# Kernel optimization log

Measured on AMD Instinct MI355X. Metric: run time of the kernel, lower is better.

The kernel has to match this reference:

```python
import jax, jax.numpy as jnp
import numpy as np

N, E, B = 20000, 320000, 64          # nodes, edges (before self-loops), graphs
IN_D, HID, HEADS, OUT_D = 768, 128, 4, 256
H1 = HID * HEADS                      # 512, concat output of first two GAT layers


def setup_inputs() -> dict:
    key = jax.random.key(0)
    ks = jax.random.split(key, 16)
    g = lambda k, shape, fan: jax.random.normal(k, shape, jnp.float32) * (1.0 / np.sqrt(fan))
    x = jax.random.normal(ks[0], (N, IN_D), jnp.float32)
    edge_index = jax.random.randint(ks[1], (2, E), 0, N)
    batch = jnp.sort(jax.random.randint(ks[2], (N,), 0, B))
    return {
        "x": x, "edge_index": edge_index, "batch": batch,
        # layer 1: in 768 -> 4 heads x 128, concat
        "W1": g(ks[3], (IN_D, H1), IN_D), "a_src1": g(ks[4], (HEADS, HID), HID),
        "a_dst1": g(ks[5], (HEADS, HID), HID), "b1": jnp.zeros((H1,), jnp.float32),
        "gamma1": jnp.ones((H1,), jnp.float32), "beta1": jnp.zeros((H1,), jnp.float32),
        # layer 2: in 512 -> 4 heads x 128, concat
        "W2": g(ks[6], (H1, H1), H1), "a_src2": g(ks[7], (HEADS, HID), HID),
        "a_dst2": g(ks[8], (HEADS, HID), HID), "b2": jnp.zeros((H1,), jnp.float32),
        "gamma2": jnp.ones((H1,), jnp.float32), "beta2": jnp.zeros((H1,), jnp.float32),
        # layer 3: in 512 -> 1 head x 256, no concat
        "W3": g(ks[9], (H1, OUT_D), H1), "a_src3": g(ks[10], (1, OUT_D), OUT_D),
        "a_dst3": g(ks[11], (1, OUT_D), OUT_D), "b3": jnp.zeros((OUT_D,), jnp.float32),
    }


def _gat(h_in, src, dst, W, a_s, a_d, b, heads, out_ch, concat):
    """PyG-style GATConv (shared src/dst weight, leaky_relu(0.2) attention)."""
    n = h_in.shape[0]
    h = (h_in @ W).reshape(n, heads, out_ch)                       # [N,H,C]
    e = jax.nn.leaky_relu(jnp.sum(h * a_s, -1)[src] + jnp.sum(h * a_d, -1)[dst], 0.2)  # [E,H]
    m = jax.ops.segment_max(e, dst, num_segments=n)                # stable segment softmax over dst
    p = jnp.exp(e - m[dst])
    alpha = p / (jax.ops.segment_sum(p, dst, num_segments=n)[dst] + 1e-16)
    out = jax.ops.segment_sum(h[src] * alpha[:, :, None], dst, num_segments=n)  # [N,H,C]
    out = out.reshape(n, heads * out_ch) if concat else out.mean(1)
    return out + b


def _bn(x, gamma, beta):
    mu = jnp.mean(x, axis=0)
    var = jnp.var(x, axis=0)
    return gamma * (x - mu) / jnp.sqrt(var + 1e-5) + beta


def reference(x, edge_index, batch,
              W1, a_src1, a_dst1, b1, gamma1, beta1,
              W2, a_src2, a_dst2, b2, gamma2, beta2,
              W3, a_src3, a_dst3, b3):
    loops = jnp.arange(N, dtype=edge_index.dtype)                  # PyG adds self-loops
    src = jnp.concatenate([edge_index[0], loops])
    dst = jnp.concatenate([edge_index[1], loops])
    h = _gat(x, src, dst, W1, a_src1, a_dst1, b1, HEADS, HID, True)
    h = jax.nn.leaky_relu(_bn(h, gamma1, beta1), 0.2)
    h = _gat(h, src, dst, W2, a_src2, a_dst2, b2, HEADS, HID, True)
    h = jax.nn.leaky_relu(_bn(h, gamma2, beta2), 0.2)
    h = jax.nn.leaky_relu(_gat(h, src, dst, W3, a_src3, a_dst3, b3, 1, OUT_D, False), 0.2)
    # global mean pool per graph
    sums = jax.ops.segment_sum(h, batch, num_segments=B)           # [B,OUT_D]
    cnt = jax.ops.segment_sum(jnp.ones((N, 1), h.dtype), batch, num_segments=B)
    return sums / jnp.maximum(cnt, 1.0)
```

## Files before the change

### kernel.cpp

```cpp
#include <hip/hip_runtime.h>
#include <hip/hip_bf16.h>

typedef __hip_bfloat16 bf16;
#define DEV __device__ __forceinline__

using short8 = __attribute__((ext_vector_type(8))) short;
using f32x4  = __attribute__((ext_vector_type(4))) float;

constexpr int NN   = 20000;
constexpr int NE   = 320000;
constexpr int ET   = NE + NN;
constexpr int NB   = 64;
constexpr int IND  = 768;
constexpr int HID  = 128;
constexpr int NH   = 4;
constexpr int H1   = 512;
constexpr int OUTD = 256;
constexpr int NBLK = (NN + 255) / 256;

DEV float b2f(bf16 v) { return __bfloat162float(v); }
DEV bf16  f2b(float v) { return __float2bfloat16(v); }
DEV short f2bs(float v) { bf16 h = __float2bfloat16(v); return *reinterpret_cast<short*>(&h); }
DEV float us2f(unsigned short u) { bf16 h; *reinterpret_cast<unsigned short*>(&h) = u; return __bfloat162float(h); }
DEV float lrelu(float x) { return x > 0.f ? x : 0.2f * x; }

DEV short8 load8(const bf16* p) { return *reinterpret_cast<const short8*>(p); }
DEV short8 load8(const float* p) {
  const float4 a = *reinterpret_cast<const float4*>(p);
  const float4 b = *reinterpret_cast<const float4*>(p + 4);
  short8 r;
  r[0] = f2bs(a.x); r[1] = f2bs(a.y); r[2] = f2bs(a.z); r[3] = f2bs(a.w);
  r[4] = f2bs(b.x); r[5] = f2bs(b.y); r[6] = f2bs(b.z); r[7] = f2bs(b.w);
  return r;
}

__global__ __launch_bounds__(256) void wt_kernel(
    const float* __restrict__ W, bf16* __restrict__ wt, int K, int N)
{
  __shared__ float tile[32][33];
  const int k0 = blockIdx.x * 32;
  const int n0 = blockIdx.y * 32;
  const int tx = threadIdx.x & 31;
  const int ty0 = threadIdx.x >> 5;
  for (int ty = ty0; ty < 32; ty += 8)
    tile[ty][tx] = W[(size_t)(k0 + ty) * N + n0 + tx];
  __syncthreads();
  for (int ty = ty0; ty < 32; ty += 8)
    wt[(size_t)(n0 + ty) * K + k0 + tx] = f2b(tile[tx][ty]);
}

template <typename T>
__global__ __launch_bounds__(256) void gemm_mfma(
    const T* __restrict__ A, const bf16* __restrict__ Wt,
    bf16* __restrict__ C, int M, int K, int N)
{
  __shared__ char lds[2 * 128 * 64 * 2];
  char* Asw = lds;
  char* Bsw = lds + 16384;
  const int t    = threadIdx.x;
  const int lane = t & 63;
  const int wid  = t >> 6;
  const int wr   = wid >> 1, wc = wid & 1;
  const int brow = blockIdx.x * 128;
  const int bcol = blockIdx.y * 128;
  const int l15  = lane & 15;
  const int kq   = (lane >> 4) * 8;

  f32x4 acc[4][4];
#pragma unroll
  for (int m = 0; m < 4; ++m)
#pragma unroll
    for (int n = 0; n < 4; ++n) acc[m][n] = (f32x4){0.f, 0.f, 0.f, 0.f};

  for (int kt = 0; kt < K; kt += 64) {
#pragma unroll
    for (int i = 0; i < 4; ++i) {
      const int idx = i * 256 + t;
      const int row = idx >> 3;
      const int k8  = (idx & 7) * 8;
      const int woff = (row * 128 + k8 * 2) ^ ((row & 7) << 4);
      short8 av = {0, 0, 0, 0, 0, 0, 0, 0};
      if (brow + row < M) av = load8(A + (size_t)(brow + row) * K + kt + k8);
      *reinterpret_cast<short8*>(Asw + woff) = av;
      const short8 bv = load8(Wt + (size_t)(bcol + row) * K + kt + k8);
      *reinterpret_cast<short8*>(Bsw + woff) = bv;
    }
    __syncthreads();
#pragma unroll
    for (int kk = 0; kk < 2; ++kk) {
      short8 a[4], b[4];
#pragma unroll
      for (int m = 0; m < 4; ++m) {
        const int r = wr * 64 + m * 16 + l15;
        const int k = kk * 32 + kq;
        a[m] = *reinterpret_cast<const short8*>(Asw + ((r * 128 + k * 2) ^ ((r & 7) << 4)));
      }
#pragma unroll
      for (int n = 0; n < 4; ++n) {
        const int r = wc * 64 + n * 16 + l15;
        const int k = kk * 32 + kq;
        b[n] = *reinterpret_cast<const short8*>(Bsw + ((r * 128 + k * 2) ^ ((r & 7) << 4)));
      }
#pragma unroll
      for (int m = 0; m < 4; ++m)
#pragma unroll
        for (int n = 0; n < 4; ++n)
          acc[m][n] = __builtin_amdgcn_mfma_f32_16x16x32_bf16(a[m], b[n], acc[m][n], 0, 0, 0);
    }
    __syncthreads();
  }
#pragma unroll
  for (int m = 0; m < 4; ++m) {
    const int rbase = brow + wr * 64 + m * 16 + (lane >> 4) * 4;
#pragma unroll
    for (int r = 0; r < 4; ++r) {
      const int row = rbase + r;
      if (row < M) {
#pragma unroll
        for (int n = 0; n < 4; ++n) {
          const int col = bcol + wc * 64 + n * 16 + l15;
          C[(size_t)row * N + col] = f2b(acc[m][n][r]);
        }
      }
    }
  }
}

__global__ __launch_bounds__(256) void scores_kernel(
    const bf16* __restrict__ h, const float* __restrict__ a_src, const float* __restrict__ a_dst,
    float* __restrict__ ssrc, float* __restrict__ sdst, int H, int C)
{
  const int n = blockIdx.x;
  const int t = threadIdx.x;
  __shared__ float red[2][4];
  const bf16* hrow = h + (size_t)n * H * C;
  for (int hd = 0; hd < H; ++hd) {
    float as_ = 0.f, ad_ = 0.f;
    for (int c = t; c < C; c += 256) {
      const float hv = b2f(hrow[hd * C + c]);
      as_ += hv * a_src[hd * C + c];
      ad_ += hv * a_dst[hd * C + c];
    }
#pragma unroll
    for (int off = 32; off; off >>= 1) { as_ += __shfl_down(as_, off); ad_ += __shfl_down(ad_, off); }
    const int wid = t >> 6, lane = t & 63;
    if (lane == 0) { red[0][wid] = as_; red[1][wid] = ad_; }
    __syncthreads();
    if (t == 0) {
      ssrc[n * H + hd] = red[0][0] + red[0][1] + red[0][2] + red[0][3];
      sdst[n * H + hd] = red[1][0] + red[1][1] + red[1][2] + red[1][3];
    }
    __syncthreads();
  }
}

DEV void edge_sd(const int* __restrict__ ei, int e, int& s, int& d) {
  if (e < NE) { s = ei[e]; d = ei[NE + e]; } else { s = d = e - NE; }
}

__global__ void deg_count_kernel(const int* __restrict__ ei, int* __restrict__ deg)
{
  const int e = blockIdx.x * blockDim.x + threadIdx.x;
  if (e >= ET) return;
  int s, d; edge_sd(ei, e, s, d);
  atomicAdd(&deg[d], 1);
}

__global__ __launch_bounds__(256) void scan_p1_kernel(
    const int* __restrict__ deg, int* __restrict__ bsum)
{
  __shared__ int red[4];
  const int i = blockIdx.x * 256 + threadIdx.x;
  int v = (i < NN) ? deg[i] : 0;
#pragma unroll
  for (int off = 32; off; off >>= 1) v += __shfl_down(v, off);
  if ((threadIdx.x & 63) == 0) red[threadIdx.x >> 6] = v;
  __syncthreads();
  if (threadIdx.x == 0) bsum[blockIdx.x] = red[0] + red[1] + red[2] + red[3];
}

__global__ __launch_bounds__(128) void scan_p2_kernel(
    const int* __restrict__ bsum, int* __restrict__ boff)
{
  __shared__ int buf[128];
  const int t = threadIdx.x;
  const int v = (t < NBLK) ? bsum[t] : 0;
  buf[t] = v;
  __syncthreads();
  for (int off = 1; off < 128; off <<= 1) {
    const int add = (t >= off) ? buf[t - off] : 0;
    __syncthreads();
    buf[t] += add;
    __syncthreads();
  }
  if (t < NBLK) boff[t] = buf[t] - v;
}

__global__ __launch_bounds__(256) void scan_p3_kernel(
    const int* __restrict__ deg, const int* __restrict__ boff,
    int* __restrict__ rowptr, int* __restrict__ cursor)
{
  __shared__ int buf[256];
  const int t = threadIdx.x;
  const int i = blockIdx.x * 256 + t;
  const int v = (i < NN) ? deg[i] : 0;
  buf[t] = v;
  __syncthreads();
  for (int off = 1; off < 256; off <<= 1) {
    const int add = (t >= off) ? buf[t - off] : 0;
    __syncthreads();
    buf[t] += add;
    __syncthreads();
  }
  if (i < NN) {
    const int incl = boff[blockIdx.x] + buf[t];
    rowptr[i + 1] = incl;
    cursor[i]     = incl - v;
  }
  if (blockIdx.x == 0 && t == 0) rowptr[0] = 0;
}

__global__ void scatter_kernel(const int* __restrict__ ei, int* __restrict__ cursor,
                               int* __restrict__ esrc)
{
  const int e = blockIdx.x * blockDim.x + threadIdx.x;
  if (e >= ET) return;
  int s, d; edge_sd(ei, e, s, d);
  const int pos = atomicAdd(&cursor[d], 1);
  esrc[pos] = s;
}

template <int H, int C>
__global__ __launch_bounds__(256) void gat_agg_fused(
    const int* __restrict__ rowptr, const int* __restrict__ esrc,
    const bf16* __restrict__ h, const float* __restrict__ ssrc,
    const float* __restrict__ sdst, const float* __restrict__ bias,
    float* __restrict__ agg)
{
  constexpr int D = H * C;
  const int d  = blockIdx.x;
  const int t  = threadIdx.x;
  const int c0 = 2 * t;
  const int hd = c0 / C;
  __shared__ float sdl[H];
  __shared__ float smax[H];
  __shared__ float ssum[H];
  __shared__ int   ech[64];
  __shared__ float ep[64 * H];
  if (t < H) { sdl[t] = sdst[d * H + t]; smax[t] = -3.4e38f; ssum[t] = 0.f; }
  const int e0 = rowptr[d], e1 = rowptr[d + 1];
  __syncthreads();
  for (int base = e0; base < e1; base += 64) {
    const int m = min(64, e1 - base);
    if (t < m) ech[t] = esrc[base + t];
    __syncthreads();
    if (t < m * H) {
      const int i  = t / H;
      const int hh = t - i * H;
      ep[t] = lrelu(ssrc[ech[i] * H + hh] + sdl[hh]);
    }
    __syncthreads();
    if (t < H) {
      float mx = smax[t];
      for (int i = 0; i < m; ++i) mx = fmaxf(mx, ep[i * H + t]);
      smax[t] = mx;
    }
    __syncthreads();
  }
  float a0 = 0.f, a1 = 0.f;
  for (int base = e0; base < e1; base += 64) {
    const int m = min(64, e1 - base);
    if (t < m) ech[t] = esrc[base + t];
    __syncthreads();
    if (t < m * H) {
      const int i  = t / H;
      const int hh = t - i * H;
      ep[t] = __expf(lrelu(ssrc[ech[i] * H + hh] + sdl[hh]) - smax[hh]);
    }
    __syncthreads();
    if (t < H) {
      float s = ssum[t];
      for (int i = 0; i < m; ++i) s += ep[i * H + t];
      ssum[t] = s;
    }
    for (int i = 0; i < m; ++i) {
      const int s = ech[i];
      const unsigned hv = *reinterpret_cast<const unsigned*>(h + (size_t)s * D + c0);
      const float p = ep[i * H + hd];
      a0 += p * us2f((unsigned short)(hv & 0xffffu));
      a1 += p * us2f((unsigned short)(hv >> 16));
    }
    __syncthreads();
  }
  __syncthreads();
  const float inv = 1.f / (ssum[hd] + 1e-16f);
  agg[(size_t)d * D + c0]     = bias[c0]     + a0 * inv;
  agg[(size_t)d * D + c0 + 1] = bias[c0 + 1] + a1 * inv;
}

__global__ __launch_bounds__(512) void bn_stats_kernel(
    const float* __restrict__ x, float* __restrict__ sum, float* __restrict__ sq)
{
  const int c = threadIdx.x;
  const int r0 = blockIdx.x * 256;
  const int r1 = min(r0 + 256, NN);
  float s = 0.f, q = 0.f;
  for (int r = r0; r < r1; ++r) { const float v = x[(size_t)r * H1 + c]; s += v; q += v * v; }
  atomicAdd(&sum[c], s);
  atomicAdd(&sq[c], q);
}

__global__ void bn_final_kernel(const float* __restrict__ sum, const float* __restrict__ sq,
                                const float* __restrict__ gamma, const float* __restrict__ beta,
                                float* __restrict__ scale, float* __restrict__ shift)
{
  const int c = blockIdx.x * blockDim.x + threadIdx.x;
  if (c >= H1) return;
  const float mean = sum[c] / (float)NN;
  const float var  = sq[c] / (float)NN - mean * mean;
  const float sc   = gamma[c] / sqrtf(var + 1e-5f);
  scale[c] = sc;
  shift[c] = beta[c] - mean * sc;
}

__global__ void bn_apply_kernel(const float* __restrict__ x, const float* __restrict__ scale,
                                const float* __restrict__ shift, bf16* __restrict__ outp, int total)
{
  for (int i = blockIdx.x * blockDim.x + threadIdx.x; i < total; i += gridDim.x * blockDim.x) {
    const int c = i & (H1 - 1);
    outp[i] = f2b(lrelu(x[i] * scale[c] + shift[c]));
  }
}

__global__ __launch_bounds__(256) void pool2_kernel(
    const float* __restrict__ agg3, const int* __restrict__ batch,
    float* __restrict__ psum, int* __restrict__ pcnt)
{
  const int n0 = blockIdx.x * 64;
  const int m  = min(64, NN - n0);
  const int t  = threadIdx.x;
  __shared__ int sb[64];
  if (t < m) sb[t] = batch[n0 + t];
  __syncthreads();
  float acc = 0.f;
  int cur = sb[0], cnt = 0;
  for (int i = 0; i < m; ++i) {
    const int b = sb[i];
    if (b != cur) {
      atomicAdd(&psum[cur * OUTD + t], acc);
      if (t == 0) atomicAdd(&pcnt[cur], cnt);
      acc = 0.f; cnt = 0; cur = b;
    }
    acc += lrelu(agg3[(size_t)(n0 + i) * OUTD + t]);
    ++cnt;
  }
  atomicAdd(&psum[cur * OUTD + t], acc);
  if (t == 0) atomicAdd(&pcnt[cur], cnt);
}

__global__ void pool_out_kernel(const float* __restrict__ psum, const int* __restrict__ pcnt,
                                float* __restrict__ out)
{
  const int i = blockIdx.x * blockDim.x + threadIdx.x;
  if (i >= NB * OUTD) return;
  const int b = i / OUTD;
  const float cnt = (float)max(pcnt[b], 1);
  out[i] = psum[i] / cnt;
}

extern "C" void kernel_launch(void* const* d_in, const int* in_sizes, int n_in,
                              void* d_out, int out_size, void* d_ws, size_t ws_size,
                              hipStream_t stream)
{
  const float* x   = (const float*)d_in[0];
  const int*   ei  = (const int*)  d_in[1];
  const int*   bat = (const int*)  d_in[2];
  const float* W1  = (const float*)d_in[3];
  const float* as1 = (const float*)d_in[4];
  const float* ad1 = (const float*)d_in[5];
  const float* b1  = (const float*)d_in[6];
  const float* g1  = (const float*)d_in[7];
  const float* be1 = (const float*)d_in[8];
  const float* W2  = (const float*)d_in[9];
  const float* as2 = (const float*)d_in[10];
  const float* ad2 = (const float*)d_in[11];
  const float* b2  = (const float*)d_in[12];
  const float* g2  = (const float*)d_in[13];
  const float* be2 = (const float*)d_in[14];
  const float* W3  = (const float*)d_in[15];
  const float* as3 = (const float*)d_in[16];
  const float* ad3 = (const float*)d_in[17];
  const float* b3  = (const float*)d_in[18];
  float* out = (float*)d_out;

  char* w = (char*)d_ws;
  auto alloc = [&](size_t bytes) { void* p = (void*)w; w += (bytes + 511) & ~(size_t)511; return p; };
  bf16*     buf0   = (bf16*)    alloc((size_t)NN * H1 * 2);
  bf16*     buf1   = (bf16*)    alloc((size_t)NN * H1 * 2);
  float*    agg    = (float*)   alloc((size_t)NN * H1 * 4);
  float*    ssrc   = (float*)   alloc((size_t)NN * NH * 4);
  float*    sdst   = (float*)   alloc((size_t)NN * NH * 4);
  int*      deg    = (int*)     alloc((size_t)NN * 4);
  int*      rowptr = (int*)     alloc((size_t)(NN + 1) * 4);
  int*      cursor = (int*)     alloc((size_t)NN * 4);
  int*      bsum   = (int*)     alloc((size_t)NBLK * 4);
  int*      boff   = (int*)     alloc((size_t)NBLK * 4);
  int*      esrc   = (int*)     alloc((size_t)ET * 4);
  bf16*     wt1    = (bf16*)    alloc((size_t)H1 * IND * 2);
  bf16*     wt2    = (bf16*)    alloc((size_t)H1 * H1 * 2);
  bf16*     wt3    = (bf16*)    alloc((size_t)OUTD * H1 * 2);
  float*    bnsum  = (float*)   alloc(H1 * 4);
  float*    bnsq   = (float*)   alloc(H1 * 4);
  float*    bnsc   = (float*)   alloc(H1 * 4);
  float*    bnsh   = (float*)   alloc(H1 * 4);
  float*    psum   = (float*)   alloc(NB * OUTD * 4);
  int*      pcnt   = (int*)     alloc(NB * 4);

  { dim3 g(IND / 32, H1 / 32);  wt_kernel<<<g, 256, 0, stream>>>(W1, wt1, IND, H1); }
  { dim3 g(H1 / 32,  H1 / 32);  wt_kernel<<<g, 256, 0, stream>>>(W2, wt2, H1,  H1); }
  { dim3 g(H1 / 32, OUTD / 32); wt_kernel<<<g, 256, 0, stream>>>(W3, wt3, H1, OUTD); }
  hipMemsetAsync(deg, 0, (size_t)NN * 4, stream);
  deg_count_kernel<<<(ET + 255) / 256, 256, 0, stream>>>(ei, deg);
  scan_p1_kernel<<<NBLK, 256, 0, stream>>>(deg, bsum);
  scan_p2_kernel<<<1, 128, 0, stream>>>(bsum, boff);
  scan_p3_kernel<<<NBLK, 256, 0, stream>>>(deg, boff, rowptr, cursor);
  scatter_kernel<<<(ET + 255) / 256, 256, 0, stream>>>(ei, cursor, esrc);

  auto run_bn = [&](const float* gamma, const float* beta) {
    hipMemsetAsync(bnsum, 0, H1 * 4, stream);
    hipMemsetAsync(bnsq,  0, H1 * 4, stream);
    bn_stats_kernel<<<(NN + 255) / 256, 512, 0, stream>>>(agg, bnsum, bnsq);
    bn_final_kernel<<<2, 256, 0, stream>>>(bnsum, bnsq, gamma, beta, bnsc, bnsh);
    bn_apply_kernel<<<2048, 256, 0, stream>>>(agg, bnsc, bnsh, buf1, NN * H1);
  };

  const int gm = (NN + 127) / 128;
  { dim3 g(gm, H1 / 128);  gemm_mfma<float><<<g, 256, 0, stream>>>(x,    wt1, buf0, NN, IND, H1); }
  scores_kernel<<<NN, 256, 0, stream>>>(buf0, as1, ad1, ssrc, sdst, NH, HID);
  gat_agg_fused<NH, HID><<<NN, H1 / 2, 0, stream>>>(rowptr, esrc, buf0, ssrc, sdst, b1, agg);
  run_bn(g1, be1);
  { dim3 g(gm, H1 / 128);  gemm_mfma<bf16><<<g, 256, 0, stream>>>(buf1, wt2, buf0, NN, H1, H1); }
  scores_kernel<<<NN, 256, 0, stream>>>(buf0, as2, ad2, ssrc, sdst, NH, HID);
  gat_agg_fused<NH, HID><<<NN, H1 / 2, 0, stream>>>(rowptr, esrc, buf0, ssrc, sdst, b2, agg);
  run_bn(g2, be2);
  { dim3 g(gm, OUTD / 128); gemm_mfma<bf16><<<g, 256, 0, stream>>>(buf1, wt3, buf0, NN, H1, OUTD); }
  scores_kernel<<<NN, 256, 0, stream>>>(buf0, as3, ad3, ssrc, sdst, 1, OUTD);
  gat_agg_fused<1, OUTD><<<NN, OUTD / 2, 0, stream>>>(rowptr, esrc, buf0, ssrc, sdst, b3, agg);
  hipMemsetAsync(psum, 0, NB * OUTD * 4, stream);
  hipMemsetAsync(pcnt, 0, NB * 4, stream);
  pool2_kernel<<<(NN + 63) / 64, 256, 0, stream>>>(agg, bat, psum, pcnt);
  pool_out_kernel<<<(NB * OUTD + 255) / 256, 256, 0, stream>>>(psum, pcnt, out);
}
```

Baseline: 722.5 us.

## Aggregate GAT neighbors with one wavefront per node, no shared memory

Replaces the block-per-destination aggregation, which staged edges through shared memory with many __syncthreads, with a kernel that assigns one 64-lane wavefront to each destination node. Each lane redundantly recomputes its head's softmax max and sum from the edge scores and accumulates 8 (or 4) channels with a single vector load per edge. This removes barriers and shared-memory traffic and packs four nodes into each block. In exchange every lane does redundant score loads and exp work, and the softmax runs serially over edges within each lane.

```diff
diff --git a/kernel.cpp b/kernel.cpp
--- a/kernel.cpp
+++ b/kernel.cpp
@@ -231,71 +231,51 @@
 }
 
 template <int H, int C>
-__global__ __launch_bounds__(256) void gat_agg_fused(
+__global__ __launch_bounds__(256) void gat_agg_wave(
     const int* __restrict__ rowptr, const int* __restrict__ esrc,
     const bf16* __restrict__ h, const float* __restrict__ ssrc,
     const float* __restrict__ sdst, const float* __restrict__ bias,
     float* __restrict__ agg)
 {
-  constexpr int D = H * C;
-  const int d  = blockIdx.x;
-  const int t  = threadIdx.x;
-  const int c0 = 2 * t;
-  const int hd = c0 / C;
-  __shared__ float sdl[H];
-  __shared__ float smax[H];
-  __shared__ float ssum[H];
-  __shared__ int   ech[64];
-  __shared__ float ep[64 * H];
-  if (t < H) { sdl[t] = sdst[d * H + t]; smax[t] = -3.4e38f; ssum[t] = 0.f; }
+  constexpr int D   = H * C;
+  constexpr int CPL = D / 64;
+  const int wid  = threadIdx.x >> 6;
+  const int lane = threadIdx.x & 63;
+  const int d    = blockIdx.x * 4 + wid;
+  if (d >= NN) return;
+  const int cbase = lane * CPL;
+  const int hd    = cbase / C;
+  const float sdl = sdst[d * H + hd];
   const int e0 = rowptr[d], e1 = rowptr[d + 1];
-  __syncthreads();
-  for (int base = e0; base < e1; base += 64) {
-    const int m = min(64, e1 - base);
-    if (t < m) ech[t] = esrc[base + t];
-    __syncthreads();
-    if (t < m * H) {
-      const int i  = t / H;
-      const int hh = t - i * H;
-      ep[t] = lrelu(ssrc[ech[i] * H + hh] + sdl[hh]);
-    }
-    __syncthreads();
-    if (t < H) {
-      float mx = smax[t];
-      for (int i = 0; i < m; ++i) mx = fmaxf(mx, ep[i * H + t]);
-      smax[t] = mx;
-    }
-    __syncthreads();
-  }
-  float a0 = 0.f, a1 = 0.f;
-  for (int base = e0; base < e1; base += 64) {
-    const int m = min(64, e1 - base);
-    if (t < m) ech[t] = esrc[base + t];
-    __syncthreads();
-    if (t < m * H) {
-      const int i  = t / H;
-      const int hh = t - i * H;
-      ep[t] = __expf(lrelu(ssrc[ech[i] * H + hh] + sdl[hh]) - smax[hh]);
-    }
-    __syncthreads();
-    if (t < H) {
-      float s = ssum[t];
-      for (int i = 0; i < m; ++i) s += ep[i * H + t];
-      ssum[t] = s;
-    }
-    for (int i = 0; i < m; ++i) {
-      const int s = ech[i];
-      const unsigned hv = *reinterpret_cast<const unsigned*>(h + (size_t)s * D + c0);
-      const float p = ep[i * H + hd];
-      a0 += p * us2f((unsigned short)(hv & 0xffffu));
-      a1 += p * us2f((unsigned short)(hv >> 16));
-    }
-    __syncthreads();
-  }
-  __syncthreads();
-  const float inv = 1.f / (ssum[hd] + 1e-16f);
-  agg[(size_t)d * D + c0]     = bias[c0]     + a0 * inv;
-  agg[(size_t)d * D + c0 + 1] = bias[c0 + 1] + a1 * inv;
+  float mx = -3.4e38f;
+  for (int e = e0; e < e1; ++e) {
+    const int s = esrc[e];
+    mx = fmaxf(mx, lrelu(ssrc[s * H + hd] + sdl));
+  }
+  float acc[CPL];
+#pragma unroll
+  for (int c = 0; c < CPL; ++c) acc[c] = 0.f;
+  float psum = 0.f;
+  for (int e = e0; e < e1; ++e) {
+    const int s = esrc[e];
+    const float p = __expf(lrelu(ssrc[s * H + hd] + sdl) - mx);
+    psum += p;
+    const bf16* hp = h + (size_t)s * D + cbase;
+    if constexpr (CPL == 8) {
+      const short8 hv = *reinterpret_cast<const short8*>(hp);
+#pragma unroll
+      for (int c = 0; c < 8; ++c) acc[c] += p * us2f((unsigned short)hv[c]);
+    } else {
+      const ushort4 hv = *reinterpret_cast<const ushort4*>(hp);
+      acc[0] += p * us2f(hv.x); acc[1] += p * us2f(hv.y);
+      acc[2] += p * us2f(hv.z); acc[3] += p * us2f(hv.w);
+    }
+  }
+  const float inv = 1.f / (psum + 1e-16f);
+  float* op = agg + (size_t)d * D + cbase;
+  const float* bp = bias + cbase;
+#pragma unroll
+  for (int c = 0; c < CPL; ++c) op[c] = bp[c] + acc[c] * inv;
 }
 
 __global__ __launch_bounds__(512) void bn_stats_kernel(
@@ -435,17 +415,18 @@
   };
 
   const int gm = (NN + 127) / 128;
+  const int ga = (NN + 3) / 4;
   { dim3 g(gm, H1 / 128);  gemm_mfma<float><<<g, 256, 0, stream>>>(x,    wt1, buf0, NN, IND, H1); }
   scores_kernel<<<NN, 256, 0, stream>>>(buf0, as1, ad1, ssrc, sdst, NH, HID);
-  gat_agg_fused<NH, HID><<<NN, H1 / 2, 0, stream>>>(rowptr, esrc, buf0, ssrc, sdst, b1, agg);
+  gat_agg_wave<NH, HID><<<ga, 256, 0, stream>>>(rowptr, esrc, buf0, ssrc, sdst, b1, agg);
   run_bn(g1, be1);
   { dim3 g(gm, H1 / 128);  gemm_mfma<bf16><<<g, 256, 0, stream>>>(buf1, wt2, buf0, NN, H1, H1); }
   scores_kernel<<<NN, 256, 0, stream>>>(buf0, as2, ad2, ssrc, sdst, NH, HID);
-  gat_agg_fused<NH, HID><<<NN, H1 / 2, 0, stream>>>(rowptr, esrc, buf0, ssrc, sdst, b2, agg);
+  gat_agg_wave<NH, HID><<<ga, 256, 0, stream>>>(rowptr, esrc, buf0, ssrc, sdst, b2, agg);
   run_bn(g2, be2);
   { dim3 g(gm, OUTD / 128); gemm_mfma<bf16><<<g, 256, 0, stream>>>(buf1, wt3, buf0, NN, H1, OUTD); }
   scores_kernel<<<NN, 256, 0, stream>>>(buf0, as3, ad3, ssrc, sdst, 1, OUTD);
-  gat_agg_fused<1, OUTD><<<NN, OUTD / 2, 0, stream>>>(rowptr, esrc, buf0, ssrc, sdst, b3, agg);
+  gat_agg_wave<1, OUTD><<<ga, 256, 0, stream>>>(rowptr, esrc, buf0, ssrc, sdst, b3, agg);
   hipMemsetAsync(psum, 0, NB * OUTD * 4, stream);
   hipMemsetAsync(pcnt, 0, NB * 4, stream);
   pool2_kernel<<<(NN + 63) / 64, 256, 0, stream>>>(agg, bat, psum, pcnt);
```

Result: slower. 761.9 us (+5.5%).
